# Optimization experiments

Measured on AMD Instinct MI355X. Metric: run time of the kernel, lower is better.

The kernel has to match this reference:

```python
import jax, jax.numpy as jnp
import numpy as np
from jax import lax

B, L, H = 32, 4096, 512  # batch, v_len (encoder frames), hidden_dim


def setup_inputs() -> dict:
    key = jax.random.key(0)
    ks = jax.random.split(key, 9)
    return {
        "query": jax.random.normal(ks[0], (B, 1, H), dtype=jnp.float32),
        "value": jax.random.normal(ks[1], (B, L, H), dtype=jnp.float32),
        "last_attn": jax.random.uniform(ks[2], (B, L), dtype=jnp.float32),
        # conv1d: in_channels=1, out_channels=H, kernel_size=3
        "conv_w": jax.random.normal(ks[3], (H, 1, 3), dtype=jnp.float32) * 0.1,
        "conv_b": jax.random.normal(ks[4], (H,), dtype=jnp.float32) * 0.1,
        "Wq": jax.random.normal(ks[5], (H, H), dtype=jnp.float32) / np.sqrt(H),
        "Wv": jax.random.normal(ks[6], (H, H), dtype=jnp.float32) / np.sqrt(H),
        "Ws": jax.random.normal(ks[7], (H,), dtype=jnp.float32) / np.sqrt(H),  # score_proj weight (1,H) flattened
        "bs": jnp.zeros((), dtype=jnp.float32),  # score_proj bias
        "bias": jax.random.uniform(ks[8], (H,), minval=-0.1, maxval=0.1, dtype=jnp.float32),
    }


def reference(query, value, last_attn, conv_w, conv_b, Wq, Wv, Ws, bs, bias):
    # conv1d over previous alignment: (B,1,L) -> (B,H,L), then transpose to (B,L,H)
    conv_attn = lax.conv_general_dilated(
        last_attn[:, None, :], conv_w, window_strides=(1,), padding=[(1, 1)],
        dimension_numbers=("NCH", "OIH", "NCH"))
    conv_attn = conv_attn.transpose(0, 2, 1) + conv_b[None, None, :]  # (B,L,H)

    q = jnp.einsum("bqh,oh->bqo", query, Wq)   # (B,1,H), broadcasts over L
    v = jnp.einsum("blh,oh->blo", value, Wv)   # (B,L,H)
    e = jnp.tanh(q + v + conv_attn + bias)     # (B,L,H)
    score = jnp.einsum("blh,h->bl", e, Ws) + bs  # (B,L)

    # smoothing=True branch: sigmoid + sum-normalize
    score = jax.nn.sigmoid(score)
    attn = score / jnp.sum(score, axis=-1, keepdims=True)  # (B,L)

    context = jnp.einsum("bl,blh->bh", attn, value)  # (B,H)
    out = jnp.concatenate([context, query[:, 0, :]], axis=1)  # (B,2H)
    return out, attn
```

## Files before the change

### kernel.cpp

```cpp
#include <hip/hip_runtime.h>
#include <hip/hip_bf16.h>
#include <math.h>

#define BB 32
#define LL 4096
#define HH 512
#define TM 64

typedef __attribute__((ext_vector_type(8))) short short8;
typedef __attribute__((ext_vector_type(8))) unsigned short u16x8;
typedef __attribute__((ext_vector_type(4))) float f32x4;

__device__ __forceinline__ unsigned short f2bf(float f) {
  __hip_bfloat16 h = __float2bfloat16(f);
  unsigned short u;
  __builtin_memcpy(&u, &h, 2);
  return u;
}
__device__ __forceinline__ float bf2f(unsigned short u) {
  unsigned int x = ((unsigned int)u) << 16;
  float f;
  __builtin_memcpy(&f, &x, 4);
  return f;
}
__device__ __forceinline__ float fast_tanh(float x) {
  float e = __expf(2.f * x);
  return 1.f - 2.f / (e + 1.f);
}

__global__ __launch_bounds__(256) void prep_base(
    const float* __restrict__ query, const float* __restrict__ Wq,
    const float* __restrict__ bias, const float* __restrict__ conv_b,
    float* __restrict__ base) {
  const int b = blockIdx.x >> 1;
  const int o = ((blockIdx.x & 1) << 8) + threadIdx.x;
  __shared__ float qrow[HH];
  for (int i = threadIdx.x; i < HH; i += 256) qrow[i] = query[b * HH + i];
  __syncthreads();
  const float* wq = Wq + (size_t)o * HH;
  float acc = 0.f;
  for (int h = 0; h < HH; h += 4) {
    float4 w = *(const float4*)(wq + h);
    acc += w.x * qrow[h] + w.y * qrow[h + 1] + w.z * qrow[h + 2] + w.w * qrow[h + 3];
  }
  base[b * HH + o] = acc + bias[o] + conv_b[o];
}

__global__ __launch_bounds__(256) void prep_wv(const float* __restrict__ Wv,
                                               unsigned short* __restrict__ wvf) {
  const int chunk = blockIdx.x * 256 + threadIdx.x;
  const int l = chunk & 63;
  const int kk = (chunk >> 6) & 15;
  const int nb = chunk >> 10;
  const int row = nb * 16 + (l & 15);
  const int colf = kk * 32 + (l >> 4) * 8;
  const float* src = Wv + (size_t)row * HH + colf;
  u16x8 v;
  #pragma unroll
  for (int j = 0; j < 8; ++j) v[j] = f2bf(src[j]);
  *(u16x8*)(wvf + (size_t)chunk * 8) = v;
}

__global__ __launch_bounds__(512, 4) void main_kernel(
    const float* __restrict__ value, const float* __restrict__ last_attn,
    const float* __restrict__ conv_w, const unsigned short* __restrict__ wvf,
    const float* __restrict__ Ws, const float* __restrict__ bs,
    const float* __restrict__ base, float* __restrict__ ctx,
    float* __restrict__ attn) {
  const int b = blockIdx.y;
  const int l0 = blockIdx.x * TM;
  const int tid = threadIdx.x;
  const int w = tid >> 6;
  const int lane = tid & 63;

  __shared__ __align__(16) unsigned short A[TM * HH];
  __shared__ float la_s[TM + 2];
  __shared__ float scorered[8][TM];
  __shared__ float srow[TM];

  char* Ab = (char*)A;

  const float* vsrc = value + (size_t)(b * LL + l0) * HH;
  #pragma unroll
  for (int i = 0; i < 8; ++i) {
    const int c = tid + i * 512;
    const int row = c >> 6;
    const int cb = c & 63;
    const float4* s4 = (const float4*)(vsrc + (size_t)row * HH + cb * 8);
    float4 lo = s4[0], hi = s4[1];
    u16x8 v;
    v[0] = f2bf(lo.x); v[1] = f2bf(lo.y); v[2] = f2bf(lo.z); v[3] = f2bf(lo.w);
    v[4] = f2bf(hi.x); v[5] = f2bf(hi.y); v[6] = f2bf(hi.z); v[7] = f2bf(hi.w);
    const int off = row * 1024 + ((cb * 16) ^ ((row & 7) << 4));
    *(u16x8*)(Ab + off) = v;
  }
  if (tid < TM + 2) {
    int l = l0 - 1 + tid;
    la_s[tid] = (l >= 0 && l < LL) ? last_attn[b * LL + l] : 0.f;
  }
  __syncthreads();

  f32x4 acc[4][4] = {};
  const int g = lane >> 4;
  const int r16 = lane & 15;

  short8 bcur[4], bnxt[4];
  #pragma unroll
  for (int n = 0; n < 4; ++n)
    bcur[n] = *(const short8*)(wvf + ((size_t)((w * 4 + n) * 16 + 0) * 64 + lane) * 8);

  for (int kk = 0; kk < 16; ++kk) {
    if (kk < 15) {
      #pragma unroll
      for (int n = 0; n < 4; ++n)
        bnxt[n] = *(const short8*)(wvf + ((size_t)((w * 4 + n) * 16 + kk + 1) * 64 + lane) * 8);
    }
    #pragma unroll
    for (int m = 0; m < 4; ++m) {
      const int row = m * 16 + r16;
      const int off = row * 1024 + ((kk * 64 + g * 16) ^ ((row & 7) << 4));
      short8 a = *(const short8*)(Ab + off);
      #pragma unroll
      for (int n = 0; n < 4; ++n)
        acc[m][n] = __builtin_amdgcn_mfma_f32_16x16x32_bf16(a, bcur[n], acc[m][n], 0, 0, 0);
    }
    #pragma unroll
    for (int n = 0; n < 4; ++n) bcur[n] = bnxt[n];
  }

  float basev[4], wsv[4], cw0[4], cw1[4], cw2[4];
  #pragma unroll
  for (int n = 0; n < 4; ++n) {
    const int col = w * 64 + n * 16 + r16;
    basev[n] = base[b * HH + col];
    wsv[n] = Ws[col];
    cw0[n] = conv_w[col * 3 + 0];
    cw1[n] = conv_w[col * 3 + 1];
    cw2[n] = conv_w[col * 3 + 2];
  }
  #pragma unroll
  for (int m = 0; m < 4; ++m) {
    #pragma unroll
    for (int j = 0; j < 4; ++j) {
      const int row = m * 16 + g * 4 + j;
      const float lam = la_s[row], laz = la_s[row + 1], lap = la_s[row + 2];
      float sum = 0.f;
      #pragma unroll
      for (int n = 0; n < 4; ++n) {
        float e = acc[m][n][j] + basev[n] + cw0[n] * lam + cw1[n] * laz + cw2[n] * lap;
        sum += fast_tanh(e) * wsv[n];
      }
      sum += __shfl_xor(sum, 1, 64);
      sum += __shfl_xor(sum, 2, 64);
      sum += __shfl_xor(sum, 4, 64);
      sum += __shfl_xor(sum, 8, 64);
      if (r16 == 0) scorered[w][row] = sum;
    }
  }
  __syncthreads();
  if (tid < TM) {
    float sc = bs[0];
    #pragma unroll
    for (int ww = 0; ww < 8; ++ww) sc += scorered[ww][tid];
    float s = 1.f / (1.f + __expf(-sc));
    srow[tid] = s;
    attn[b * LL + l0 + tid] = s;
  }
  __syncthreads();

  const int rg = tid & 7;
  const int cc = tid >> 3;
  float cs[8];
  #pragma unroll
  for (int k = 0; k < 8; ++k) cs[k] = 0.f;
  #pragma unroll
  for (int i = 0; i < 8; ++i) {
    const int row = rg * 8 + i;
    const int off = row * 1024 + ((cc * 16) ^ ((row & 7) << 4));
    u16x8 v = *(const u16x8*)(Ab + off);
    const float s = srow[row];
    #pragma unroll
    for (int k = 0; k < 8; ++k) cs[k] += s * bf2f(v[k]);
  }
  #pragma unroll
  for (int o = 1; o < 8; o <<= 1) {
    #pragma unroll
    for (int k = 0; k < 8; ++k) cs[k] += __shfl_xor(cs[k], o, 64);
  }
  if (rg == 0) {
    #pragma unroll
    for (int k = 0; k < 8; ++k) atomicAdd(&ctx[b * HH + cc * 8 + k], cs[k]);
  }
}

__global__ __launch_bounds__(512) void finalize_kernel(
    const float* __restrict__ query, const float* __restrict__ ctx,
    float* __restrict__ out, float* __restrict__ attn) {
  const int b = blockIdx.x;
  const int tid = threadIdx.x;
  __shared__ float red[8];
  float s = 0.f;
  for (int l = tid; l < LL; l += 512) s += attn[b * LL + l];
  #pragma unroll
  for (int off = 32; off > 0; off >>= 1) s += __shfl_xor(s, off, 64);
  if ((tid & 63) == 0) red[tid >> 6] = s;
  __syncthreads();
  float S = 0.f;
  #pragma unroll
  for (int i = 0; i < 8; ++i) S += red[i];
  const float inv = 1.f / S;
  out[b * 2 * HH + tid] = ctx[b * HH + tid] * inv;
  out[b * 2 * HH + HH + tid] = query[b * HH + tid];
  for (int l = tid; l < LL; l += 512) attn[b * LL + l] *= inv;
}

extern "C" void kernel_launch(void* const* d_in, const int* in_sizes, int n_in,
                              void* d_out, int out_size, void* d_ws, size_t ws_size,
                              hipStream_t stream) {
  const float* query     = (const float*)d_in[0];
  const float* value     = (const float*)d_in[1];
  const float* last_attn = (const float*)d_in[2];
  const float* conv_w    = (const float*)d_in[3];
  const float* conv_b    = (const float*)d_in[4];
  const float* Wq        = (const float*)d_in[5];
  const float* Wv        = (const float*)d_in[6];
  const float* Ws        = (const float*)d_in[7];
  const float* bs        = (const float*)d_in[8];
  const float* bias      = (const float*)d_in[9];

  float* out  = (float*)d_out;
  float* attn = out + BB * 2 * HH;
  float* base = (float*)d_ws;
  float* ctx  = base + BB * HH;
  unsigned short* wvf = (unsigned short*)(ctx + BB * HH);

  hipMemsetAsync(ctx, 0, BB * HH * sizeof(float), stream);
  prep_base<<<64, 256, 0, stream>>>(query, Wq, bias, conv_b, base);
  prep_wv<<<128, 256, 0, stream>>>(Wv, wvf);
  dim3 grid(LL / TM, BB);
  main_kernel<<<grid, 512, 0, stream>>>(value, last_attn, conv_w, wvf, Ws, bs,
                                        base, ctx, attn);
  finalize_kernel<<<BB, 512, 0, stream>>>(query, ctx, out, attn);
}
```

Baseline: 212.0 us.

## Stream value tiles directly from global memory instead of staging bf16 copy in LDS

Drops the 64KB LDS staging of the bf16-converted value tile. Each wave now loads its MFMA A-fragments straight from global memory (or cache) and converts them in registers. The context pass re-reads value in fp32 and reduces partial sums through a small shared buffer before the atomics. This cuts LDS use, which should allow more resident blocks and overlap of loads with MFMA. In exchange, all 8 waves fetch the same value tile redundantly from global/L2 and the tile is read again for the context.

```diff
diff --git a/kernel.cpp b/kernel.cpp
--- a/kernel.cpp
+++ b/kernel.cpp
@@ -16,12 +16,6 @@
   unsigned short u;
   __builtin_memcpy(&u, &h, 2);
   return u;
-}
-__device__ __forceinline__ float bf2f(unsigned short u) {
-  unsigned int x = ((unsigned int)u) << 16;
-  float f;
-  __builtin_memcpy(&f, &x, 4);
-  return f;
 }
 __device__ __forceinline__ float fast_tanh(float x) {
   float e = __expf(2.f * x);
@@ -72,37 +66,26 @@
   const int tid = threadIdx.x;
   const int w = tid >> 6;
   const int lane = tid & 63;
-
-  __shared__ __align__(16) unsigned short A[TM * HH];
+  const int g = lane >> 4;
+  const int r16 = lane & 15;
+
   __shared__ float la_s[TM + 2];
   __shared__ float scorered[8][TM];
   __shared__ float srow[TM];
-
-  char* Ab = (char*)A;
-
-  const float* vsrc = value + (size_t)(b * LL + l0) * HH;
-  #pragma unroll
-  for (int i = 0; i < 8; ++i) {
-    const int c = tid + i * 512;
-    const int row = c >> 6;
-    const int cb = c & 63;
-    const float4* s4 = (const float4*)(vsrc + (size_t)row * HH + cb * 8);
-    float4 lo = s4[0], hi = s4[1];
-    u16x8 v;
-    v[0] = f2bf(lo.x); v[1] = f2bf(lo.y); v[2] = f2bf(lo.z); v[3] = f2bf(lo.w);
-    v[4] = f2bf(hi.x); v[5] = f2bf(hi.y); v[6] = f2bf(hi.z); v[7] = f2bf(hi.w);
-    const int off = row * 1024 + ((cb * 16) ^ ((row & 7) << 4));
-    *(u16x8*)(Ab + off) = v;
-  }
+  __shared__ float ctxred[8][HH];
+
   if (tid < TM + 2) {
     int l = l0 - 1 + tid;
     la_s[tid] = (l >= 0 && l < LL) ? last_attn[b * LL + l] : 0.f;
   }
   __syncthreads();
 
+  const float* abase[4];
+  #pragma unroll
+  for (int m = 0; m < 4; ++m)
+    abase[m] = value + (size_t)(b * LL + l0 + m * 16 + r16) * HH + g * 8;
+
   f32x4 acc[4][4] = {};
-  const int g = lane >> 4;
-  const int r16 = lane & 15;
 
   short8 bcur[4], bnxt[4];
   #pragma unroll
@@ -115,11 +98,20 @@
       for (int n = 0; n < 4; ++n)
         bnxt[n] = *(const short8*)(wvf + ((size_t)((w * 4 + n) * 16 + kk + 1) * 64 + lane) * 8);
     }
+    float4 lo[4], hi[4];
     #pragma unroll
     for (int m = 0; m < 4; ++m) {
-      const int row = m * 16 + r16;
-      const int off = row * 1024 + ((kk * 64 + g * 16) ^ ((row & 7) << 4));
-      short8 a = *(const short8*)(Ab + off);
+      const float* p = abase[m] + kk * 32;
+      lo[m] = *(const float4*)(p);
+      hi[m] = *(const float4*)(p + 4);
+    }
+    #pragma unroll
+    for (int m = 0; m < 4; ++m) {
+      short8 a;
+      a[0] = (short)f2bf(lo[m].x); a[1] = (short)f2bf(lo[m].y);
+      a[2] = (short)f2bf(lo[m].z); a[3] = (short)f2bf(lo[m].w);
+      a[4] = (short)f2bf(hi[m].x); a[5] = (short)f2bf(hi[m].y);
+      a[6] = (short)f2bf(hi[m].z); a[7] = (short)f2bf(hi[m].w);
       #pragma unroll
       for (int n = 0; n < 4; ++n)
         acc[m][n] = __builtin_amdgcn_mfma_f32_16x16x32_bf16(a, bcur[n], acc[m][n], 0, 0, 0);
@@ -168,28 +160,29 @@
   }
   __syncthreads();
 
-  const int rg = tid & 7;
-  const int cc = tid >> 3;
-  float cs[8];
-  #pragma unroll
-  for (int k = 0; k < 8; ++k) cs[k] = 0.f;
-  #pragma unroll
-  for (int i = 0; i < 8; ++i) {
-    const int row = rg * 8 + i;
-    const int off = row * 1024 + ((cc * 16) ^ ((row & 7) << 4));
-    u16x8 v = *(const u16x8*)(Ab + off);
-    const float s = srow[row];
-    #pragma unroll
-    for (int k = 0; k < 8; ++k) cs[k] += s * bf2f(v[k]);
-  }
-  #pragma unroll
-  for (int o = 1; o < 8; o <<= 1) {
-    #pragma unroll
-    for (int k = 0; k < 8; ++k) cs[k] += __shfl_xor(cs[k], o, 64);
-  }
-  if (rg == 0) {
-    #pragma unroll
-    for (int k = 0; k < 8; ++k) atomicAdd(&ctx[b * HH + cc * 8 + k], cs[k]);
+  {
+    float cs0 = 0.f, cs1 = 0.f, cs2 = 0.f, cs3 = 0.f;
+    float cs4 = 0.f, cs5 = 0.f, cs6 = 0.f, cs7 = 0.f;
+    #pragma unroll
+    for (int i = 0; i < 8; ++i) {
+      const int row = w * 8 + i;
+      const float* p = value + (size_t)(b * LL + l0 + row) * HH + lane * 8;
+      float4 lo = *(const float4*)(p);
+      float4 hi = *(const float4*)(p + 4);
+      const float s = srow[row];
+      cs0 += s * lo.x; cs1 += s * lo.y; cs2 += s * lo.z; cs3 += s * lo.w;
+      cs4 += s * hi.x; cs5 += s * hi.y; cs6 += s * hi.z; cs7 += s * hi.w;
+    }
+    float* r = &ctxred[w][lane * 8];
+    r[0] = cs0; r[1] = cs1; r[2] = cs2; r[3] = cs3;
+    r[4] = cs4; r[5] = cs5; r[6] = cs6; r[7] = cs7;
+  }
+  __syncthreads();
+  {
+    float sum = 0.f;
+    #pragma unroll
+    for (int ww = 0; ww < 8; ++ww) sum += ctxred[ww][tid];
+    atomicAdd(&ctx[b * HH + tid], sum);
   }
 }
 
```

Measured after the change: 326.2 us. +53.9%, slower.

## Halve row tile, raise occupancy, fuse prep kernels and reduce ctx in LDS

Applied to the files above, without the earlier changes.

Halves the rows per block from 64 to 32, which doubles the grid and shrinks the shared A tile. The launch-bounds occupancy hint rises from 4 to 6. The B-operand register double buffering is dropped in favour of direct loads inside the k loop. The memset and two prep kernels are merged into one launch that also zeroes ctx. Context accumulation now reduces across warps in LDS and issues one atomic per column per block, instead of shuffles plus per-thread atomics. The aim is higher occupancy and fewer launches, but every block now reloads the full Wv fragments and there are twice as many ctx atomics overall.

```diff
diff --git a/kernel.cpp b/kernel.cpp
--- a/kernel.cpp
+++ b/kernel.cpp
@@ -5,7 +5,7 @@
 #define BB 32
 #define LL 4096
 #define HH 512
-#define TM 64
+#define TM 32
 
 typedef __attribute__((ext_vector_type(8))) short short8;
 typedef __attribute__((ext_vector_type(8))) unsigned short u16x8;
@@ -28,40 +28,42 @@
   return 1.f - 2.f / (e + 1.f);
 }
 
-__global__ __launch_bounds__(256) void prep_base(
+__global__ __launch_bounds__(256) void prep_kernel(
     const float* __restrict__ query, const float* __restrict__ Wq,
     const float* __restrict__ bias, const float* __restrict__ conv_b,
-    float* __restrict__ base) {
-  const int b = blockIdx.x >> 1;
-  const int o = ((blockIdx.x & 1) << 8) + threadIdx.x;
-  __shared__ float qrow[HH];
-  for (int i = threadIdx.x; i < HH; i += 256) qrow[i] = query[b * HH + i];
-  __syncthreads();
-  const float* wq = Wq + (size_t)o * HH;
-  float acc = 0.f;
-  for (int h = 0; h < HH; h += 4) {
-    float4 w = *(const float4*)(wq + h);
-    acc += w.x * qrow[h] + w.y * qrow[h + 1] + w.z * qrow[h + 2] + w.w * qrow[h + 3];
-  }
-  base[b * HH + o] = acc + bias[o] + conv_b[o];
-}
-
-__global__ __launch_bounds__(256) void prep_wv(const float* __restrict__ Wv,
-                                               unsigned short* __restrict__ wvf) {
-  const int chunk = blockIdx.x * 256 + threadIdx.x;
-  const int l = chunk & 63;
-  const int kk = (chunk >> 6) & 15;
-  const int nb = chunk >> 10;
-  const int row = nb * 16 + (l & 15);
-  const int colf = kk * 32 + (l >> 4) * 8;
-  const float* src = Wv + (size_t)row * HH + colf;
-  u16x8 v;
-  #pragma unroll
-  for (int j = 0; j < 8; ++j) v[j] = f2bf(src[j]);
-  *(u16x8*)(wvf + (size_t)chunk * 8) = v;
-}
-
-__global__ __launch_bounds__(512, 4) void main_kernel(
+    const float* __restrict__ Wv, float* __restrict__ base,
+    unsigned short* __restrict__ wvf, float* __restrict__ ctx) {
+  const int bid = blockIdx.x;
+  if (bid < 64) {
+    const int b = bid >> 1;
+    const int o = ((bid & 1) << 8) + threadIdx.x;
+    __shared__ float qrow[HH];
+    for (int i = threadIdx.x; i < HH; i += 256) qrow[i] = query[b * HH + i];
+    __syncthreads();
+    const float* wq = Wq + (size_t)o * HH;
+    float acc = 0.f;
+    for (int h = 0; h < HH; h += 4) {
+      float4 w = *(const float4*)(wq + h);
+      acc += w.x * qrow[h] + w.y * qrow[h + 1] + w.z * qrow[h + 2] + w.w * qrow[h + 3];
+    }
+    base[b * HH + o] = acc + bias[o] + conv_b[o];
+    ctx[b * HH + o] = 0.f;
+  } else {
+    const int chunk = (bid - 64) * 256 + threadIdx.x;
+    const int l = chunk & 63;
+    const int kk = (chunk >> 6) & 15;
+    const int nb = chunk >> 10;
+    const int row = nb * 16 + (l & 15);
+    const int colf = kk * 32 + (l >> 4) * 8;
+    const float* src = Wv + (size_t)row * HH + colf;
+    u16x8 v;
+    #pragma unroll
+    for (int j = 0; j < 8; ++j) v[j] = f2bf(src[j]);
+    *(u16x8*)(wvf + (size_t)chunk * 8) = v;
+  }
+}
+
+__global__ __launch_bounds__(512, 6) void main_kernel(
     const float* __restrict__ value, const float* __restrict__ last_attn,
     const float* __restrict__ conv_w, const unsigned short* __restrict__ wvf,
     const float* __restrict__ Ws, const float* __restrict__ bs,
@@ -72,17 +74,20 @@
   const int tid = threadIdx.x;
   const int w = tid >> 6;
   const int lane = tid & 63;
+  const int g = lane >> 4;
+  const int r16 = lane & 15;
 
   __shared__ __align__(16) unsigned short A[TM * HH];
   __shared__ float la_s[TM + 2];
   __shared__ float scorered[8][TM];
   __shared__ float srow[TM];
+  __shared__ float ctxred[8][HH];
 
   char* Ab = (char*)A;
 
   const float* vsrc = value + (size_t)(b * LL + l0) * HH;
   #pragma unroll
-  for (int i = 0; i < 8; ++i) {
+  for (int i = 0; i < 4; ++i) {
     const int c = tid + i * 512;
     const int row = c >> 6;
     const int cb = c & 63;
@@ -100,32 +105,19 @@
   }
   __syncthreads();
 
-  f32x4 acc[4][4] = {};
-  const int g = lane >> 4;
-  const int r16 = lane & 15;
-
-  short8 bcur[4], bnxt[4];
-  #pragma unroll
-  for (int n = 0; n < 4; ++n)
-    bcur[n] = *(const short8*)(wvf + ((size_t)((w * 4 + n) * 16 + 0) * 64 + lane) * 8);
-
+  f32x4 acc[2][4] = {};
+  #pragma unroll 2
   for (int kk = 0; kk < 16; ++kk) {
-    if (kk < 15) {
-      #pragma unroll
-      for (int n = 0; n < 4; ++n)
-        bnxt[n] = *(const short8*)(wvf + ((size_t)((w * 4 + n) * 16 + kk + 1) * 64 + lane) * 8);
-    }
-    #pragma unroll
-    for (int m = 0; m < 4; ++m) {
-      const int row = m * 16 + r16;
-      const int off = row * 1024 + ((kk * 64 + g * 16) ^ ((row & 7) << 4));
-      short8 a = *(const short8*)(Ab + off);
-      #pragma unroll
-      for (int n = 0; n < 4; ++n)
-        acc[m][n] = __builtin_amdgcn_mfma_f32_16x16x32_bf16(a, bcur[n], acc[m][n], 0, 0, 0);
-    }
-    #pragma unroll
-    for (int n = 0; n < 4; ++n) bcur[n] = bnxt[n];
+    const int co = kk * 64 + g * 16;
+    const int row0 = r16, row1 = 16 + r16;
+    short8 a0 = *(const short8*)(Ab + row0 * 1024 + (co ^ ((row0 & 7) << 4)));
+    short8 a1 = *(const short8*)(Ab + row1 * 1024 + (co ^ ((row1 & 7) << 4)));
+    #pragma unroll
+    for (int n = 0; n < 4; ++n) {
+      short8 bf = *(const short8*)(wvf + ((size_t)((w * 4 + n) * 16 + kk) * 64 + lane) * 8);
+      acc[0][n] = __builtin_amdgcn_mfma_f32_16x16x32_bf16(a0, bf, acc[0][n], 0, 0, 0);
+      acc[1][n] = __builtin_amdgcn_mfma_f32_16x16x32_bf16(a1, bf, acc[1][n], 0, 0, 0);
+    }
   }
 
   float basev[4], wsv[4], cw0[4], cw1[4], cw2[4];
@@ -139,7 +131,7 @@
     cw2[n] = conv_w[col * 3 + 2];
   }
   #pragma unroll
-  for (int m = 0; m < 4; ++m) {
+  for (int m = 0; m < 2; ++m) {
     #pragma unroll
     for (int j = 0; j < 4; ++j) {
       const int row = m * 16 + g * 4 + j;
@@ -168,28 +160,29 @@
   }
   __syncthreads();
 
-  const int rg = tid & 7;
-  const int cc = tid >> 3;
-  float cs[8];
-  #pragma unroll
-  for (int k = 0; k < 8; ++k) cs[k] = 0.f;
-  #pragma unroll
-  for (int i = 0; i < 8; ++i) {
-    const int row = rg * 8 + i;
-    const int off = row * 1024 + ((cc * 16) ^ ((row & 7) << 4));
-    u16x8 v = *(const u16x8*)(Ab + off);
-    const float s = srow[row];
-    #pragma unroll
-    for (int k = 0; k < 8; ++k) cs[k] += s * bf2f(v[k]);
-  }
-  #pragma unroll
-  for (int o = 1; o < 8; o <<= 1) {
-    #pragma unroll
-    for (int k = 0; k < 8; ++k) cs[k] += __shfl_xor(cs[k], o, 64);
-  }
-  if (rg == 0) {
-    #pragma unroll
-    for (int k = 0; k < 8; ++k) atomicAdd(&ctx[b * HH + cc * 8 + k], cs[k]);
+  {
+    float cs[8];
+    #pragma unroll
+    for (int k = 0; k < 8; ++k) cs[k] = 0.f;
+    #pragma unroll
+    for (int i = 0; i < 4; ++i) {
+      const int row = w * 4 + i;
+      const int off = row * 1024 + ((lane * 16) ^ ((row & 7) << 4));
+      u16x8 v = *(const u16x8*)(Ab + off);
+      const float s = srow[row];
+      #pragma unroll
+      for (int k = 0; k < 8; ++k) cs[k] += s * bf2f(v[k]);
+    }
+    float* r = &ctxred[w][lane * 8];
+    #pragma unroll
+    for (int k = 0; k < 8; ++k) r[k] = cs[k];
+  }
+  __syncthreads();
+  {
+    float sum = 0.f;
+    #pragma unroll
+    for (int ww = 0; ww < 8; ++ww) sum += ctxred[ww][tid];
+    atomicAdd(&ctx[b * HH + tid], sum);
   }
 }
 
@@ -234,9 +227,7 @@
   float* ctx  = base + BB * HH;
   unsigned short* wvf = (unsigned short*)(ctx + BB * HH);
 
-  hipMemsetAsync(ctx, 0, BB * HH * sizeof(float), stream);
-  prep_base<<<64, 256, 0, stream>>>(query, Wq, bias, conv_b, base);
-  prep_wv<<<128, 256, 0, stream>>>(Wv, wvf);
+  prep_kernel<<<192, 256, 0, stream>>>(query, Wq, bias, conv_b, Wv, base, wvf, ctx);
   dim3 grid(LL / TM, BB);
   main_kernel<<<grid, 512, 0, stream>>>(value, last_attn, conv_w, wvf, Ws, bs,
                                         base, ctx, attn);
```

Result: faster. 185.3 us (-12.6%).
